# Kernel optimization log

Measured on AMD Instinct MI355X. Metric: run time of the kernel, lower is better.

Reference implementation:

```python
import jax, jax.numpy as jnp
import numpy as np
import math

B, S, D, H = 2, 2048, 1024, 16
DK = D // H


def setup_inputs() -> dict:
    key = jax.random.key(0)
    ks = jax.random.split(key, 12)
    scale = 1.0 / math.sqrt(D)
    inp = {
        "query": jax.random.normal(ks[0], (B, S, D), jnp.float32),
        "key": jax.random.normal(ks[1], (B, S, D), jnp.float32),
        "value": jax.random.normal(ks[2], (B, S, D), jnp.float32),
        # causal 0/1 mask, broadcast over heads
        "mask": jnp.broadcast_to(jnp.tril(jnp.ones((S, S), jnp.int32)), (B, 1, S, S)),
        "Wq": jax.random.normal(ks[3], (D, D), jnp.float32) * scale,
        "bq": jnp.zeros((D,), jnp.float32),
        "Wk": jax.random.normal(ks[4], (D, D), jnp.float32) * scale,
        "bk": jnp.zeros((D,), jnp.float32),
        "Wv": jax.random.normal(ks[5], (D, D), jnp.float32) * scale,
        "bv": jnp.zeros((D,), jnp.float32),
        "Wo": jax.random.normal(ks[6], (D, D), jnp.float32) * scale,
        "bo": jnp.zeros((D,), jnp.float32),
    }
    return inp


def _split_heads(x):
    # [B,S,D] -> [B,H,S,DK]
    return x.reshape(B, S, H, DK).transpose(0, 2, 1, 3)


def reference(query, key, value, mask, Wq, bq, Wk, bk, Wv, bv, Wo, bo):
    q = _split_heads(query @ Wq.T + bq)
    k = _split_heads(key @ Wk.T + bk)
    v = _split_heads(value @ Wv.T + bv)
    # scaled dot-product attention with additive mask (mask==0 -> -inf)
    scores = jnp.einsum("bhqd,bhkd->bhqk", q, k) / math.sqrt(DK)
    scores = jnp.where(mask == 0, -jnp.inf, scores)
    w = jax.nn.softmax(scores, axis=-1)
    out = jnp.einsum("bhqk,bhkd->bhqd", w, v)
    out = out.transpose(0, 2, 1, 3).reshape(B, S, D)
    return out @ Wo.T + bo
```

## Files before the change

kernel.cpp:

```cpp
#include <hip/hip_runtime.h>
#include <hip/hip_bf16.h>
#include <math.h>

#define BBATCH 2
#define SSEQ 2048
#define DMODEL 1024
#define NH 16
#define MTOT (BBATCH*SSEQ)

typedef short bfrag __attribute__((ext_vector_type(8)));
typedef float ffrag __attribute__((ext_vector_type(4)));
typedef float f16frag __attribute__((ext_vector_type(16)));
typedef unsigned int uiv2 __attribute__((ext_vector_type(2)));

typedef const __attribute__((address_space(1))) unsigned int* gas_t;
typedef __attribute__((address_space(3))) unsigned int* las_t;

__device__ __forceinline__ void dl16(const void* g, void* l) {
  __builtin_amdgcn_global_load_lds((gas_t)(unsigned long long)g,
                                   (las_t)(unsigned int)(unsigned long long)l,
                                   16, 0, 0);
}

__device__ __forceinline__ void drain_vm() {
  asm volatile("s_waitcnt vmcnt(0)" ::: "memory");
}

#if defined(__has_builtin) && __has_builtin(__builtin_amdgcn_exp2f)
__device__ __forceinline__ float fexp2(float x) { return __builtin_amdgcn_exp2f(x); }
#else
__device__ __forceinline__ float fexp2(float x) { return exp2f(x); }
#endif

#if defined(__has_builtin) && __has_builtin(__builtin_amdgcn_permlane32_swap)
__device__ __forceinline__ void pl32swap(unsigned &a, unsigned &b) {
  uiv2 r = __builtin_amdgcn_permlane32_swap(a, b, false, false);
  a = r[0]; b = r[1];
}
#else
__device__ __forceinline__ void pl32swap(unsigned &a, unsigned &b) {
  asm volatile("v_permlane32_swap_b32 %0, %1" : "+v"(a), "+v"(b));
}
#endif

__device__ __forceinline__ unsigned short f2bf(float f) {
  union { float f; unsigned u; } v; v.f = f;
  unsigned r = v.u + 0x7fffu + ((v.u >> 16) & 1u);
  return (unsigned short)(r >> 16);
}

__device__ __forceinline__ unsigned pkbf2(float a, float b) {
  float2 f; f.x = a; f.y = b;
  union { __hip_bfloat162 h; unsigned u; } cv;
  cv.h = __float22bfloat162_rn(f);
  return cv.u;
}

__global__ __launch_bounds__(256) void convert_all_kernel(
    const float* __restrict__ q, const float* __restrict__ k, const float* __restrict__ v,
    const float* __restrict__ wq, const float* __restrict__ wk,
    const float* __restrict__ wv, const float* __restrict__ wo,
    unsigned short* __restrict__ dst)
{
  const long NIN = (long)MTOT * DMODEL;
  const long NW  = (long)DMODEL * DMODEL;
  const long total8 = (3 * NIN + 4 * NW) >> 3;
  long i8 = (long)blockIdx.x * blockDim.x + threadIdx.x;
  const long stride = (long)gridDim.x * blockDim.x;
  for (; i8 < total8; i8 += stride) {
    const long i = i8 << 3;
    const float* src; long off;
    if (i < NIN)          { src = q; off = i; }
    else if (i < 2 * NIN) { src = k; off = i - NIN; }
    else if (i < 3 * NIN) { src = v; off = i - 2 * NIN; }
    else {
      const long j = i - 3 * NIN;
      const int wsel = (int)(j >> 20);
      off = j & (NW - 1);
      src = (wsel == 0) ? wq : (wsel == 1) ? wk : (wsel == 2) ? wv : wo;
    }
    const float4 x0 = *(const float4*)(src + off);
    const float4 x1 = *(const float4*)(src + off + 4);
    ushort4 o0, o1;
    o0.x = f2bf(x0.x); o0.y = f2bf(x0.y); o0.z = f2bf(x0.z); o0.w = f2bf(x0.w);
    o1.x = f2bf(x1.x); o1.y = f2bf(x1.y); o1.z = f2bf(x1.z); o1.w = f2bf(x1.w);
    union { ushort4 s[2]; uint4 u; } pk; pk.s[0] = o0; pk.s[1] = o1;
    *(uint4*)(dst + i) = pk.u;
  }
}

struct ProjArgs {
  const unsigned short* X[3];
  const unsigned short* W[3];
  const float* bias[3];
  unsigned short* dst[3];
  float scale[3];
};

__global__ __launch_bounds__(256, 2) void qkv_proj(ProjArgs a)
{
  __shared__ alignas(16) unsigned short As[2][128 * 64];
  __shared__ alignas(16) unsigned short Bs[2][128 * 64];
  const int t = threadIdx.x;
  const int lane = t & 63, w = t >> 6;
  const int quad = lane >> 4, l16 = lane & 15;
  const int m0 = blockIdx.x * 128;
  const int n0 = blockIdx.y * 128;
  const int z = blockIdx.z;
  const unsigned short* __restrict__ X = a.X[z];
  const unsigned short* __restrict__ W = a.W[z];
  const int wm = (w & 1) * 64, wn = (w >> 1) * 64;

  int sw[2];
#pragma unroll
  for (int c = 0; c < 2; ++c) sw[c] = (((c * 4 + quad) ^ (l16 & 7)) * 8);

  ffrag acc[4][4];
#pragma unroll
  for (int i = 0; i < 4; ++i)
#pragma unroll
    for (int j = 0; j < 4; ++j)
#pragma unroll
      for (int e = 0; e < 4; ++e) acc[i][j][e] = 0.f;

#pragma unroll
  for (int i = 0; i < 4; ++i) {
    const int ch = i * 256 + t;
    const int row = ch >> 3, lc = (ch & 7) ^ (row & 7);
    dl16(X + (size_t)(m0 + row) * DMODEL + lc * 8, As[0] + ch * 8);
    dl16(W + (size_t)(n0 + row) * DMODEL + lc * 8, Bs[0] + ch * 8);
  }

  for (int kk = 0; kk < 16; ++kk) {
    const int cur = kk & 1;
    drain_vm();
    __syncthreads();

    if (kk < 15) {
      const int k1 = (kk + 1) * 64, nxt = cur ^ 1;
#pragma unroll
      for (int i = 0; i < 4; ++i) {
        const int ch = i * 256 + t;
        const int row = ch >> 3, lc = (ch & 7) ^ (row & 7);
        dl16(X + (size_t)(m0 + row) * DMODEL + k1 + lc * 8, As[nxt] + ch * 8);
        dl16(W + (size_t)(n0 + row) * DMODEL + k1 + lc * 8, Bs[nxt] + ch * 8);
      }
    }

    bfrag af[4][2], bg[4][2];
#pragma unroll
    for (int fi = 0; fi < 4; ++fi)
#pragma unroll
      for (int c = 0; c < 2; ++c) {
        af[fi][c] = *(const bfrag*)&As[cur][(wm + fi * 16 + l16) * 64 + sw[c]];
        bg[fi][c] = *(const bfrag*)&Bs[cur][(wn + fi * 16 + l16) * 64 + sw[c]];
      }
#pragma unroll
    for (int c = 0; c < 2; ++c)
#pragma unroll
      for (int fi = 0; fi < 4; ++fi)
#pragma unroll
        for (int fj = 0; fj < 4; ++fj)
          acc[fi][fj] = __builtin_amdgcn_mfma_f32_16x16x32_bf16(af[fi][c], bg[fj][c], acc[fi][fj], 0, 0, 0);
  }

  const float sc = a.scale[z];
  const float* __restrict__ bias = a.bias[z];
  unsigned short* __restrict__ dst = a.dst[z];
#pragma unroll
  for (int fj = 0; fj < 4; ++fj) {
    const int n = n0 + wn + fj * 16 + l16;
    const float bv = bias[n];
    const int h = n >> 6, dk = n & 63;
    if (z < 2) {
#pragma unroll
      for (int fi = 0; fi < 4; ++fi)
#pragma unroll
        for (int r = 0; r < 4; ++r) {
          const int m = m0 + wm + fi * 16 + quad * 4 + r;
          const int b_ = m >> 11, s_ = m & (SSEQ - 1);
          dst[((size_t)(b_ * NH + h) * SSEQ + s_) * 64 + dk] = f2bf((acc[fi][fj][r] + bv) * sc);
        }
    } else {
#pragma unroll
      for (int fi = 0; fi < 4; ++fi) {
        const int m = m0 + wm + fi * 16 + quad * 4;
        const int b_ = m >> 11, s_ = m & (SSEQ - 1);
        const int jt = s_ >> 6, kl = s_ & 63;
        ushort4 pk;
        pk.x = f2bf(acc[fi][fj][0] + bv);
        pk.y = f2bf(acc[fi][fj][1] + bv);
        pk.z = f2bf(acc[fi][fj][2] + bv);
        pk.w = f2bf(acc[fi][fj][3] + bv);
        *(ushort4*)&dst[(((size_t)(b_ * NH + h) * 32 + jt) * 64 + dk) * 64 + kl] = pk;
      }
    }
  }
}

__global__ __launch_bounds__(256, 2) void out_proj(
    const unsigned short* __restrict__ X,
    const unsigned short* __restrict__ W,
    const float* __restrict__ bias,
    float* __restrict__ Y)
{
  __shared__ alignas(16) unsigned short As[2][128 * 64];
  __shared__ alignas(16) unsigned short Bs[2][64 * 64];
  const int t = threadIdx.x;
  const int lane = t & 63, w = t >> 6;
  const int quad = lane >> 4, l16 = lane & 15;
  const int m0 = blockIdx.x * 128;
  const int n0 = blockIdx.y * 64;
  const int wm = (w & 1) * 64, wn = (w >> 1) * 32;

  int sw[2];
#pragma unroll
  for (int c = 0; c < 2; ++c) sw[c] = (((c * 4 + quad) ^ (l16 & 7)) * 8);

  ffrag acc[4][2];
#pragma unroll
  for (int i = 0; i < 4; ++i)
#pragma unroll
    for (int j = 0; j < 2; ++j)
#pragma unroll
      for (int e = 0; e < 4; ++e) acc[i][j][e] = 0.f;

#pragma unroll
  for (int i = 0; i < 4; ++i) {
    const int ch = i * 256 + t;
    const int row = ch >> 3, lc = (ch & 7) ^ (row & 7);
    dl16(X + (size_t)(m0 + row) * DMODEL + lc * 8, As[0] + ch * 8);
  }
#pragma unroll
  for (int i = 0; i < 2; ++i) {
    const int ch = i * 256 + t;
    const int row = ch >> 3, lc = (ch & 7) ^ (row & 7);
    dl16(W + (size_t)(n0 + row) * DMODEL + lc * 8, Bs[0] + ch * 8);
  }

  for (int kk = 0; kk < 16; ++kk) {
    const int cur = kk & 1;
    drain_vm();
    __syncthreads();

    if (kk < 15) {
      const int k1 = (kk + 1) * 64, nxt = cur ^ 1;
#pragma unroll
      for (int i = 0; i < 4; ++i) {
        const int ch = i * 256 + t;
        const int row = ch >> 3, lc = (ch & 7) ^ (row & 7);
        dl16(X + (size_t)(m0 + row) * DMODEL + k1 + lc * 8, As[nxt] + ch * 8);
      }
#pragma unroll
      for (int i = 0; i < 2; ++i) {
        const int ch = i * 256 + t;
        const int row = ch >> 3, lc = (ch & 7) ^ (row & 7);
        dl16(W + (size_t)(n0 + row) * DMODEL + k1 + lc * 8, Bs[nxt] + ch * 8);
      }
    }

    bfrag af[4][2], bg[2][2];
#pragma unroll
    for (int fi = 0; fi < 4; ++fi)
#pragma unroll
      for (int c = 0; c < 2; ++c)
        af[fi][c] = *(const bfrag*)&As[cur][(wm + fi * 16 + l16) * 64 + sw[c]];
#pragma unroll
    for (int fj = 0; fj < 2; ++fj)
#pragma unroll
      for (int c = 0; c < 2; ++c)
        bg[fj][c] = *(const bfrag*)&Bs[cur][(wn + fj * 16 + l16) * 64 + sw[c]];
#pragma unroll
    for (int c = 0; c < 2; ++c)
#pragma unroll
      for (int fi = 0; fi < 4; ++fi)
#pragma unroll
        for (int fj = 0; fj < 2; ++fj)
          acc[fi][fj] = __builtin_amdgcn_mfma_f32_16x16x32_bf16(af[fi][c], bg[fj][c], acc[fi][fj], 0, 0, 0);
  }

#pragma unroll
  for (int fj = 0; fj < 2; ++fj) {
    const int n = n0 + wn + fj * 16 + l16;
    const float bv = bias[n];
#pragma unroll
    for (int fi = 0; fi < 4; ++fi)
#pragma unroll
      for (int r = 0; r < 4; ++r) {
        const int m = m0 + wm + fi * 16 + quad * 4 + r;
        Y[(size_t)m * DMODEL + n] = acc[fi][fj][r] + bv;
      }
  }
}

__global__ __launch_bounds__(512, 4) void attn_mfma(
    const unsigned short* __restrict__ Q,
    const unsigned short* __restrict__ K,
    const unsigned short* __restrict__ Vt_g,
    unsigned short* __restrict__ ctx)
{
  __shared__ alignas(16) unsigned short Kb[2][2][64 * 64];
  __shared__ alignas(16) unsigned short Vb[2][2][64 * 64];

  const int t = threadIdx.x;
  const int lane = t & 63, w = t >> 6;
  const int l31 = lane & 31, h = lane >> 5;
  const int bid = blockIdx.x;
  const int xcd = bid & 7;
  const int j_  = bid >> 3;
  const int bh = xcd * 4 + (j_ >> 4);
  const int x  = j_ & 15;
  const int qt_lo = x, qt_hi = 31 - x;
  const int qsel = w >> 2;
  const int par  = (w >> 1) & 1;
  const int qt_w = qsel ? qt_hi : qt_lo;
  const int i0_w = qt_w * 64;
  const int q0 = (w & 1) * 32;
  const int qloc = q0 + l31;
  const int b_ = bh >> 4, h_ = bh & (NH - 1);
  const int NTs = (qt_hi >> 1) + 1;

  const unsigned short* kg = K + (size_t)bh * SSEQ * 64;
  const unsigned short* vg = Vt_g + (size_t)bh * SSEQ * 64;

  const int r = t >> 3;
  const int lc = (t & 7) ^ (r & 7);
  const int goff = r * 64 + lc * 8;
  const int loff = t * 8;

  int pc[4];
#pragma unroll
  for (int ks = 0; ks < 4; ++ks) pc[ks] = ((ks * 2 + h) ^ (l31 & 7)) * 8;
  const int rb0 = l31 * 64, rb1 = (32 + l31) * 64;

#pragma unroll
  for (int p = 0; p < 2; ++p) {
    dl16(kg + p * 4096 + goff, Kb[0][p] + loff);
    dl16(vg + p * 4096 + goff, Vb[0][p] + loff);
  }

  const unsigned short* qrow = Q + ((size_t)bh * SSEQ + i0_w + qloc) * 64;
  bfrag qb[4];
#pragma unroll
  for (int ks = 0; ks < 4; ++ks)
    qb[ks] = *(const bfrag*)(qrow + ks * 16 + h * 8);

  f16frag o0, o1;
#pragma unroll
  for (int e = 0; e < 16; ++e) { o0[e] = 0.f; o1[e] = 0.f; }
  float lacc = 0.f;

  for (int st = 0; st < NTs; ++st) {
    const int cur = st & 1;
    drain_vm();
    __syncthreads();

    if (st + 1 < NTs) {
      const int nxt = cur ^ 1;
      const size_t base = (size_t)(st + 1) * 8192;
#pragma unroll
      for (int p = 0; p < 2; ++p) {
        dl16(kg + base + p * 4096 + goff, Kb[nxt][p] + loff);
        dl16(vg + base + p * 4096 + goff, Vb[nxt][p] + loff);
      }
    }

    const int jt = st * 2 + par;
    if (jt <= qt_w) {
      f16frag s0, s1;
#pragma unroll
      for (int e = 0; e < 16; ++e) { s0[e] = 0.f; s1[e] = 0.f; }
#pragma unroll
      for (int ks = 0; ks < 4; ++ks) {
        bfrag ka0 = *(const bfrag*)&Kb[cur][par][rb0 + pc[ks]];
        bfrag ka1 = *(const bfrag*)&Kb[cur][par][rb1 + pc[ks]];
        s0 = __builtin_amdgcn_mfma_f32_32x32x16_bf16(ka0, qb[ks], s0, 0, 0, 0);
        s1 = __builtin_amdgcn_mfma_f32_32x32x16_bf16(ka1, qb[ks], s1, 0, 0, 0);
      }

      const bool diag = (jt == qt_w);
      float p0[16], p1[16];
#pragma unroll
      for (int rr = 0; rr < 16; ++rr) { p0[rr] = fexp2(s0[rr]); p1[rr] = fexp2(s1[rr]); }
      if (diag) {
#pragma unroll
        for (int rr = 0; rr < 16; ++rr) {
          const int keyl = (rr & 3) + 8 * (rr >> 2) + 4 * h;
          if (keyl > qloc)      p0[rr] = 0.f;
          if (keyl + 32 > qloc) p1[rr] = 0.f;
        }
      }
      float ss = 0.f;
#pragma unroll
      for (int rr = 0; rr < 16; rr += 4)
        ss += ((p0[rr] + p0[rr + 1]) + (p0[rr + 2] + p0[rr + 3])) +
              ((p1[rr] + p1[rr + 1]) + (p1[rr + 2] + p1[rr + 3]));
      lacc += ss;

      bfrag pb[4];
#pragma unroll
      for (int ks = 0; ks < 4; ++ks) {
        const float* pp = (ks >> 1) ? p1 : p0;
        const int kb = (ks & 1) * 8;
        unsigned w0 = pkbf2(pp[kb + 0], pp[kb + 1]);
        unsigned w1 = pkbf2(pp[kb + 2], pp[kb + 3]);
        unsigned w2 = pkbf2(pp[kb + 4], pp[kb + 5]);
        unsigned w3 = pkbf2(pp[kb + 6], pp[kb + 7]);
        pl32swap(w0, w2);
        pl32swap(w1, w3);
        union { unsigned u[4]; bfrag f; } cv;
        cv.u[0] = w0; cv.u[1] = w1; cv.u[2] = w2; cv.u[3] = w3;
        pb[ks] = cv.f;
      }

#pragma unroll
      for (int ks = 0; ks < 4; ++ks) {
        bfrag va0 = *(const bfrag*)&Vb[cur][par][rb0 + pc[ks]];
        bfrag va1 = *(const bfrag*)&Vb[cur][par][rb1 + pc[ks]];
        o0 = __builtin_amdgcn_mfma_f32_32x32x16_bf16(va0, pb[ks], o0, 0, 0, 0);
        o1 = __builtin_amdgcn_mfma_f32_32x32x16_bf16(va1, pb[ks], o1, 0, 0, 0);
      }
    }
  }

  __syncthreads();
  const int mw = qsel * 2 + (w & 1);
  float* ob = (float*)&Kb[0][0][0] + mw * 2048;
  float* lb = (float*)&Vb[0][0][0] + mw * 64;
  if (par == 1) {
#pragma unroll
    for (int e = 0; e < 16; ++e) {
      ob[e * 64 + lane]        = o0[e];
      ob[(16 + e) * 64 + lane] = o1[e];
    }
    lb[lane] = lacc;
  }
  __syncthreads();
  if (par == 0) {
#pragma unroll
    for (int e = 0; e < 16; ++e) {
      o0[e] += ob[e * 64 + lane];
      o1[e] += ob[(16 + e) * 64 + lane];
    }
    lacc += lb[lane];

    const float lfull = lacc + __shfl_xor(lacc, 32, 64);
    const float inv = 1.f / lfull;
    unsigned short* cb = ctx + (size_t)(b_ * SSEQ + i0_w + qloc) * DMODEL + h_ * 64;
#pragma unroll
    for (int g = 0; g < 4; ++g) {
      const int dkb = 8 * g + 4 * h;
      union { __hip_bfloat162 hh[2]; unsigned long long u; } cv;
      float2 lo, hi;
      lo.x = o0[4 * g + 0] * inv; lo.y = o0[4 * g + 1] * inv;
      hi.x = o0[4 * g + 2] * inv; hi.y = o0[4 * g + 3] * inv;
      cv.hh[0] = __float22bfloat162_rn(lo);
      cv.hh[1] = __float22bfloat162_rn(hi);
      *(unsigned long long*)(cb + dkb) = cv.u;
      lo.x = o1[4 * g + 0] * inv; lo.y = o1[4 * g + 1] * inv;
      hi.x = o1[4 * g + 2] * inv; hi.y = o1[4 * g + 3] * inv;
      cv.hh[0] = __float22bfloat162_rn(lo);
      cv.hh[1] = __float22bfloat162_rn(hi);
      *(unsigned long long*)(cb + 32 + dkb) = cv.u;
    }
  }
}

extern "C" void kernel_launch(void* const* d_in, const int* in_sizes, int n_in,
                              void* d_out, int out_size, void* d_ws, size_t ws_size,
                              hipStream_t stream)
{
  const float* q  = (const float*)d_in[0];
  const float* k  = (const float*)d_in[1];
  const float* v  = (const float*)d_in[2];
  const float* wq = (const float*)d_in[4];
  const float* bq = (const float*)d_in[5];
  const float* wk = (const float*)d_in[6];
  const float* bk = (const float*)d_in[7];
  const float* wv = (const float*)d_in[8];
  const float* bv = (const float*)d_in[9];
  const float* wo = (const float*)d_in[10];
  const float* bo = (const float*)d_in[11];

  const long NIN = (long)MTOT * DMODEL;
  const long NW  = (long)DMODEL * DMODEL;
  unsigned short* ws16 = (unsigned short*)d_ws;
  unsigned short* qx  = ws16;
  unsigned short* kx  = qx + NIN;
  unsigned short* vx  = kx + NIN;
  unsigned short* wqb = vx + NIN;
  unsigned short* wkb = wqb + NW;
  unsigned short* wvb = wkb + NW;
  unsigned short* wob = wvb + NW;
  unsigned short* Qp  = wob + NW;
  unsigned short* Kp  = Qp + NIN;
  unsigned short* Vp  = Kp + NIN;
  unsigned short* Cx  = Vp + NIN;

  convert_all_kernel<<<2048, 256, 0, stream>>>(q, k, v, wq, wk, wv, wo, ws16);

  ProjArgs pa;
  pa.X[0] = qx;  pa.X[1] = kx;  pa.X[2] = vx;
  pa.W[0] = wqb; pa.W[1] = wkb; pa.W[2] = wvb;
  pa.bias[0] = bq; pa.bias[1] = bk; pa.bias[2] = bv;
  pa.dst[0] = Qp; pa.dst[1] = Kp; pa.dst[2] = Vp;
  pa.scale[0] = 0.18033688011112042f;
  pa.scale[1] = 1.0f;
  pa.scale[2] = 1.0f;
  qkv_proj<<<dim3(MTOT / 128, DMODEL / 128, 3), 256, 0, stream>>>(pa);

  attn_mfma<<<512, 512, 0, stream>>>(Qp, Kp, Vp, Cx);

  out_proj<<<dim3(MTOT / 128, DMODEL / 64), 256, 0, stream>>>(Cx, wob, bo, (float*)d_out);
}
```

Before: 212.5 us.

## Single-buffer K/V tiles in attention to raise occupancy

Replaces the double-buffered K/V shared-memory tiles with single buffers, which halves LDS use, and raises the launch-bounds occupancy hint from 4 to 6 blocks. The next tile's load is now issued only after a barrier at the end of each step, so global loads no longer overlap compute inside a block. The bet is that extra resident blocks hide that latency instead. The merge buffers are rearranged to fit the smaller LDS footprint, and the tighter launch bound may also limit registers per thread.

```diff
diff --git a/kernel.cpp b/kernel.cpp
--- a/kernel.cpp
+++ b/kernel.cpp
@@ -293,14 +293,15 @@
   }
 }
 
-__global__ __launch_bounds__(512, 4) void attn_mfma(
+__global__ __launch_bounds__(512, 6) void attn_mfma(
     const unsigned short* __restrict__ Q,
     const unsigned short* __restrict__ K,
     const unsigned short* __restrict__ Vt_g,
     unsigned short* __restrict__ ctx)
 {
-  __shared__ alignas(16) unsigned short Kb[2][2][64 * 64];
-  __shared__ alignas(16) unsigned short Vb[2][2][64 * 64];
+  __shared__ alignas(16) unsigned short Kb[2][64 * 64];
+  __shared__ alignas(16) unsigned short Vb[2][64 * 64];
+  __shared__ float merge_l[4][64];
 
   const int t = threadIdx.x;
   const int lane = t & 63, w = t >> 6;
@@ -335,8 +336,8 @@
 
 #pragma unroll
   for (int p = 0; p < 2; ++p) {
-    dl16(kg + p * 4096 + goff, Kb[0][p] + loff);
-    dl16(vg + p * 4096 + goff, Vb[0][p] + loff);
+    dl16(kg + p * 4096 + goff, Kb[p] + loff);
+    dl16(vg + p * 4096 + goff, Vb[p] + loff);
   }
 
   const unsigned short* qrow = Q + ((size_t)bh * SSEQ + i0_w + qloc) * 64;
@@ -351,19 +352,8 @@
   float lacc = 0.f;
 
   for (int st = 0; st < NTs; ++st) {
-    const int cur = st & 1;
     drain_vm();
     __syncthreads();
-
-    if (st + 1 < NTs) {
-      const int nxt = cur ^ 1;
-      const size_t base = (size_t)(st + 1) * 8192;
-#pragma unroll
-      for (int p = 0; p < 2; ++p) {
-        dl16(kg + base + p * 4096 + goff, Kb[nxt][p] + loff);
-        dl16(vg + base + p * 4096 + goff, Vb[nxt][p] + loff);
-      }
-    }
 
     const int jt = st * 2 + par;
     if (jt <= qt_w) {
@@ -372,8 +362,8 @@
       for (int e = 0; e < 16; ++e) { s0[e] = 0.f; s1[e] = 0.f; }
 #pragma unroll
       for (int ks = 0; ks < 4; ++ks) {
-        bfrag ka0 = *(const bfrag*)&Kb[cur][par][rb0 + pc[ks]];
-        bfrag ka1 = *(const bfrag*)&Kb[cur][par][rb1 + pc[ks]];
+        bfrag ka0 = *(const bfrag*)&Kb[par][rb0 + pc[ks]];
+        bfrag ka1 = *(const bfrag*)&Kb[par][rb1 + pc[ks]];
         s0 = __builtin_amdgcn_mfma_f32_32x32x16_bf16(ka0, qb[ks], s0, 0, 0, 0);
         s1 = __builtin_amdgcn_mfma_f32_32x32x16_bf16(ka1, qb[ks], s1, 0, 0, 0);
       }
@@ -415,25 +405,34 @@
 
 #pragma unroll
       for (int ks = 0; ks < 4; ++ks) {
-        bfrag va0 = *(const bfrag*)&Vb[cur][par][rb0 + pc[ks]];
-        bfrag va1 = *(const bfrag*)&Vb[cur][par][rb1 + pc[ks]];
+        bfrag va0 = *(const bfrag*)&Vb[par][rb0 + pc[ks]];
+        bfrag va1 = *(const bfrag*)&Vb[par][rb1 + pc[ks]];
         o0 = __builtin_amdgcn_mfma_f32_32x32x16_bf16(va0, pb[ks], o0, 0, 0, 0);
         o1 = __builtin_amdgcn_mfma_f32_32x32x16_bf16(va1, pb[ks], o1, 0, 0, 0);
       }
     }
-  }
-
-  __syncthreads();
+
+    __syncthreads();
+    if (st + 1 < NTs) {
+      const size_t base = (size_t)(st + 1) * 8192;
+#pragma unroll
+      for (int p = 0; p < 2; ++p) {
+        dl16(kg + base + p * 4096 + goff, Kb[p] + loff);
+        dl16(vg + base + p * 4096 + goff, Vb[p] + loff);
+      }
+    }
+  }
+
   const int mw = qsel * 2 + (w & 1);
-  float* ob = (float*)&Kb[0][0][0] + mw * 2048;
-  float* lb = (float*)&Vb[0][0][0] + mw * 64;
+  float* ob = (mw < 2) ? ((float*)&Kb[0][0] + mw * 2048)
+                       : ((float*)&Vb[0][0] + (mw - 2) * 2048);
   if (par == 1) {
 #pragma unroll
     for (int e = 0; e < 16; ++e) {
       ob[e * 64 + lane]        = o0[e];
       ob[(16 + e) * 64 + lane] = o1[e];
     }
-    lb[lane] = lacc;
+    merge_l[mw][lane] = lacc;
   }
   __syncthreads();
   if (par == 0) {
@@ -442,7 +441,7 @@
       o0[e] += ob[e * 64 + lane];
       o1[e] += ob[(16 + e) * 64 + lane];
     }
-    lacc += lb[lane];
+    lacc += merge_l[mw][lane];
 
     const float lfull = lacc + __shfl_xor(lacc, 32, 64);
     const float inv = 1.f / lfull;
```

After: 383.4 us. +80.4%, slower.
